# Kernel optimization log

Measured on AMD Instinct MI355X. Metric: run time of the kernel, lower is better.

The kernel has to match this reference:

```python
import jax, jax.numpy as jnp
import numpy as np

S, E, H, D, L = 2048, 1024, 16, 64, 6  # seq, embed(=H*D), heads, d_model, stack
FF = 4 * E
EPS = 1e-5


def _pos_embedding():
    pos = jnp.arange(S, dtype=jnp.float32)[:, None]
    idx = jnp.arange(E, dtype=jnp.float32)[None, :]
    ang = pos / jnp.power(10000.0, idx / E)
    # even positions -> sin row, odd positions -> cos row (as in the source)
    return jnp.where(jnp.arange(S)[:, None] % 2 == 0, jnp.sin(ang), jnp.cos(ang))


def _layer_norm(x, g, b):
    mu = jnp.mean(x, axis=-1, keepdims=True)
    var = jnp.mean(jnp.square(x - mu), axis=-1, keepdims=True)
    return (x - mu) * jax.lax.rsqrt(var + EPS) * g + b


def setup_inputs() -> dict:
    key = jax.random.key(0)
    ks = jax.random.split(key, 12)
    n = lambda k, shape, s=0.02: jax.random.normal(k, shape, jnp.float32) * s
    return {
        "x": jax.random.normal(ks[0], (S, E), jnp.float32),
        # shared (default-arg trap) input projections [d_model, embed]
        "Wk": n(ks[1], (D, E)), "Wq": n(ks[2], (D, E)), "Wv": n(ks[3], (D, E)),
        # per-layer per-head linears (stored [in,out])
        "hWk": n(ks[4], (L, H, D, D)), "hbk": jnp.zeros((L, H, D), jnp.float32),
        "hWq": n(ks[5], (L, H, D, D)), "hbq": jnp.zeros((L, H, D), jnp.float32),
        "hWv": n(ks[6], (L, H, D, D)), "hbv": jnp.zeros((L, H, D), jnp.float32),
        "Wo": n(ks[7], (L, E, E)), "bo": jnp.zeros((L, E), jnp.float32),
        "ln1_g": jnp.ones((L, E), jnp.float32), "ln1_b": jnp.zeros((L, E), jnp.float32),
        "W1": n(ks[8], (L, E, FF)), "b1": jnp.zeros((L, FF), jnp.float32),
        "W2": n(ks[9], (L, FF, E)), "b2": jnp.zeros((L, E), jnp.float32),
        "ln2_g": jnp.ones((L, E), jnp.float32), "ln2_b": jnp.zeros((L, E), jnp.float32),
    }


def reference(x, Wk, Wq, Wv, hWk, hbk, hWq, hbq, hWv, hbv, Wo, bo,
              ln1_g, ln1_b, W1, b1, W2, b2, ln2_g, ln2_b):
    h = x + _pos_embedding()
    scale = 1.0 / jnp.sqrt(jnp.float32(D))
    for l in range(L):
        # shared projections: [S, D]
        K = h @ Wk.T
        Q = h @ Wq.T
        V = h @ Wv.T
        # per-head linears: [H, S, D]
        kh = jnp.einsum('sd,hde->hse', K, hWk[l]) + hbk[l][:, None, :]
        qh = jnp.einsum('sd,hde->hse', Q, hWq[l]) + hbq[l][:, None, :]
        vh = jnp.einsum('sd,hde->hse', V, hWv[l]) + hbv[l][:, None, :]
        scores = jnp.einsum('hqd,hkd->hqk', qh, kh) * scale  # [H, S, S]
        attn = jax.nn.softmax(scores, axis=-1)
        out = jnp.einsum('hqk,hkd->hqd', attn, vh)           # [H, S, D]
        cat = jnp.transpose(out, (1, 0, 2)).reshape(S, H * D)  # [S, E]
        o = cat @ Wo[l] + bo[l]
        h = _layer_norm(o + h, ln1_g[l], ln1_b[l])
        # FFN
        f = jax.nn.relu(h @ W1[l] + b1[l]) @ W2[l] + b2[l]
        h = _layer_norm(f + h, ln2_g[l], ln2_b[l])
    return h
```

## Files before the change

### kernel.cpp

```cpp
#include <hip/hip_runtime.h>
#include <stdint.h>

typedef unsigned short u16;
typedef unsigned int   u32;

constexpr int SS = 2048, EE = 1024, HH = 16, DD = 64, LL = 6, FF = 4096;

typedef __bf16 bf16x8 __attribute__((ext_vector_type(8)));
typedef float  f32x4  __attribute__((ext_vector_type(4)));

#define DEV __device__ __forceinline__
#define AS1 __attribute__((address_space(1)))
#define AS3 __attribute__((address_space(3)))

DEV u16 f2bf(float f) {
    u32 u = __builtin_bit_cast(u32, f);
    u += 0x7FFFu + ((u >> 16) & 1u);
    return (u16)(u >> 16);
}

DEV float bf2f(u16 v) { return __builtin_bit_cast(float, (u32)v << 16); }

DEV void store_bf4(u16* p, float a, float b, float c, float d) {
    u32 lo = (u32)f2bf(a) | ((u32)f2bf(b) << 16);
    u32 hi = (u32)f2bf(c) | ((u32)f2bf(d) << 16);
    *(uint2*)p = make_uint2(lo, hi);
}

DEV void gload16(const void* g, void* l) {
    __builtin_amdgcn_global_load_lds((const AS1 void*)g, (AS3 void*)l, 16, 0, 0);
}

DEV f32x4 mfma16(bf16x8 a, bf16x8 b, f32x4 c) {
    return __builtin_amdgcn_mfma_f32_16x16x32_bf16(a, b, c, 0, 0, 0);
}

DEV float exp2_fast(float x) {
    float r;
    asm("v_exp_f32 %0, %1" : "=v"(r) : "v"(x));
    return r;
}

DEV int kvperm(int c) {
    return (c & 32) | ((c & 12) << 1) | ((c & 16) >> 2) | (c & 3);
}

DEV int xcd_swz(int flat, int nwg) {
    int chunk = nwg >> 3;
    return (flat & 7) * chunk + (flat >> 3);
}

constexpr size_t ALGN(size_t x) { return (x + 255) & ~(size_t)255; }
constexpr size_t OFF_WF   = 0;
constexpr size_t OFF_HWT  = ALGN(OFF_WF   + (size_t)3*LL*1024*1024*2);
constexpr size_t OFF_WSHT = ALGN(OFF_HWT  + (size_t)3*96*4096*2);
constexpr size_t OFF_HB   = ALGN(OFF_WSHT + (size_t)3*1024*64*2);
constexpr size_t OFF_WOT  = ALGN(OFF_HB   + (size_t)LL*3*HH*64*4);
constexpr size_t OFF_W1T  = ALGN(OFF_WOT  + (size_t)LL*EE*EE*2);
constexpr size_t OFF_W2T  = ALGN(OFF_W1T  + (size_t)LL*FF*EE*2);
constexpr size_t OFF_HBF  = ALGN(OFF_W2T  + (size_t)LL*EE*FF*2);
constexpr size_t OFF_QKVH = ALGN(OFF_HBF  + (size_t)SS*EE*2);
constexpr size_t OFF_VT   = OFF_QKVH + (size_t)2*HH*SS*64*2;
constexpr size_t OFF_CAT  = OFF_VT   + (size_t)1024*SS*2;
constexpr size_t OFF_F1   = OFF_QKVH;
constexpr size_t OFF_OF   = ALGN(OFF_CAT + (size_t)SS*EE*2);

__global__ void pos_add(const float* __restrict__ x, u16* __restrict__ hb) {
    const int row = blockIdx.x, tid = threadIdx.x;
    float4 x4 = ((const float4*)(x + (size_t)row * EE))[tid];
    float v[4] = {x4.x, x4.y, x4.z, x4.w};
    float y[4];
#pragma unroll
    for (int j = 0; j < 4; ++j) {
        int e = tid * 4 + j;
        float ang = (float)row * expf((float)e * (-9.210340371976184f / 1024.f));
        float pe = ((row & 1) == 0) ? sinf(ang) : cosf(ang);
        y[j] = v[j] + pe;
    }
    store_bf4(hb + (size_t)row * EE + tid * 4, y[0], y[1], y[2], y[3]);
}

__global__ void pack_bias(const float* __restrict__ bk, const float* __restrict__ bq,
                          const float* __restrict__ bv, float* __restrict__ dst) {
    int i = blockIdx.x * 256 + threadIdx.x;
    if (i >= LL * 3 * HH * 64) return;
    int d = i & 63;
    int hh = (i >> 6) & 15;
    int lt = i >> 10;
    int t = lt % 3, l = lt / 3;
    const float* s = (t == 0) ? bk : (t == 1) ? bq : bv;
    dst[i] = s[((size_t)l * HH + hh) * 64 + d];
}

DEV void tile_t64(const float* src, u16* dst, int R, int C, int c0, int r0,
                  float (*t)[65], int tid) {
    const int lr = tid >> 4, lc4 = (tid & 15) * 4;
#pragma unroll
    for (int i = 0; i < 4; ++i) {
        int r = i * 16 + lr;
        float4 v = *(const float4*)(src + (size_t)(r0 + r) * C + c0 + lc4);
        t[r][lc4] = v.x; t[r][lc4 + 1] = v.y; t[r][lc4 + 2] = v.z; t[r][lc4 + 3] = v.w;
    }
    __syncthreads();
    const int cr = tid >> 3, rr8 = (tid & 7) * 8;
#pragma unroll
    for (int i = 0; i < 2; ++i) {
        int cc = i * 32 + cr;
        u16 tmp[8];
#pragma unroll
        for (int j = 0; j < 8; ++j) tmp[j] = f2bf(t[rr8 + j][cc]);
        *(uint4*)(dst + (size_t)(c0 + cc) * R + r0 + rr8) = *(uint4*)tmp;
    }
}

__global__ void transpose_cast64(const float* __restrict__ src, u16* __restrict__ dst,
                                 int R, int C, long sSrc, long sDst) {
    __shared__ float t[64][65];
    const int b = blockIdx.z;
    tile_t64(src + (size_t)b * sSrc, dst + (size_t)b * sDst, R, C,
             blockIdx.x * 64, blockIdx.y * 64, t, threadIdx.x);
}

__global__ void hw_t3(const float* __restrict__ s0, const float* __restrict__ s1,
                      const float* __restrict__ s2, u16* __restrict__ dst) {
    __shared__ float t[64][65];
    const int z = blockIdx.z;
    const float* src = (z < 96 ? s0 : z < 192 ? s1 : s2) + (size_t)(z % 96) * 4096;
    tile_t64(src, dst + (size_t)z * 4096, 64, 64, 0, 0, t, threadIdx.x);
}

__global__ void wsh_t3(const float* __restrict__ s0, const float* __restrict__ s1,
                       const float* __restrict__ s2, u16* __restrict__ dst) {
    __shared__ float t[64][65];
    const int z = blockIdx.z;
    const float* src = (z == 0) ? s0 : (z == 1) ? s1 : s2;
    tile_t64(src, dst + (size_t)z * 65536, 64, 1024, blockIdx.x * 64, 0, t, threadIdx.x);
}

template<int BIASMODE, bool RELU, bool SPLITK, bool BATCH>
__launch_bounds__(256)
__global__ void gemm_std(const u16* __restrict__ A, const u16* __restrict__ B,
                         const float* __restrict__ bias, u16* __restrict__ Cb,
                         int M, int N, int K, int lda, int ldb,
                         long zsA, long zsB, long zsC) {
    __shared__ u16 As[2][128 * 64];
    __shared__ u16 Bs[2][128 * 64];
    const int gx = gridDim.x;
    const int swz = xcd_swz(blockIdx.y * gx + blockIdx.x, gx * gridDim.y);
    const int bn = swz % gx, bm = swz / gx, z = blockIdx.z;
    const int tid = threadIdx.x, w = tid >> 6;
    const int lane = tid & 63, l15 = lane & 15, hi = lane >> 4;
    const int wm = w >> 1, wn = w & 1;
    const u16* Ab = A + (size_t)bm * 128 * lda + (SPLITK ? (size_t)z * K : 0) + (BATCH ? (size_t)z * zsA : 0);
    const u16* Bb = B + (size_t)bn * 128 * ldb + (SPLITK ? (size_t)z * K : 0) + (BATCH ? (size_t)z * zsB : 0);
    const size_t coff = SPLITK ? (size_t)z * M * N : (BATCH ? (size_t)z * zsC : 0);
    const int tr = tid >> 3, tp = tid & 7;

    f32x4 acc[4][4];
#pragma unroll
    for (int i = 0; i < 4; ++i)
#pragma unroll
        for (int j = 0; j < 4; ++j) acc[i][j] = f32x4{0.f, 0.f, 0.f, 0.f};

    auto STAGE = [&](int b, int kt) {
        const u16* Abk = Ab + kt + (size_t)tr * lda + tp * 8;
        const u16* Bbk = Bb + kt + (size_t)tr * ldb + tp * 8;
#pragma unroll
        for (int i = 0; i < 4; ++i) {
            gload16(Abk + (size_t)i * 32 * lda, &As[b][(i * 256 + w * 64) * 8]);
            gload16(Bbk + (size_t)i * 32 * ldb, &Bs[b][(i * 256 + w * 64) * 8]);
        }
    };

    STAGE(0, 0);
    __syncthreads();
    int buf = 0;

    for (int kt = 0; kt < K; kt += 64) {
        if (kt + 64 < K) STAGE(buf ^ 1, kt + 64);
#pragma unroll
        for (int kk = 0; kk < 2; ++kk) {
            bf16x8 af[4], bf[4];
#pragma unroll
            for (int mi = 0; mi < 4; ++mi)
                af[mi] = *(const bf16x8*)&As[buf][(wm * 64 + mi * 16 + l15) * 64 + kk * 32 + hi * 8];
#pragma unroll
            for (int ni = 0; ni < 4; ++ni)
                bf[ni] = *(const bf16x8*)&Bs[buf][(wn * 64 + ni * 16 + l15) * 64 + kk * 32 + hi * 8];
#pragma unroll
            for (int mi = 0; mi < 4; ++mi)
#pragma unroll
                for (int ni = 0; ni < 4; ++ni)
                    acc[mi][ni] = mfma16(af[mi], bf[ni], acc[mi][ni]);
        }
        __syncthreads();
        buf ^= 1;
    }

#pragma unroll
    for (int mi = 0; mi < 4; ++mi) {
        int rg = bm * 128 + wm * 64 + mi * 16 + hi * 4;
#pragma unroll
        for (int ni = 0; ni < 4; ++ni) {
            int cg = bn * 128 + wn * 64 + ni * 16 + l15;
            float bc = (BIASMODE == 1) ? bias[cg] : 0.f;
#pragma unroll
            for (int r = 0; r < 4; ++r) {
                float v = acc[mi][ni][r] + bc;
                if (RELU) v = fmaxf(v, 0.f);
                Cb[coff + (size_t)(rg + r) * N + cg] = f2bf(v);
            }
        }
    }
}

__launch_bounds__(256)
__global__ void gemm_qkv(const u16* __restrict__ A, const u16* __restrict__ WF, int l,
                         const float* __restrict__ bias, u16* __restrict__ QKVH,
                         u16* __restrict__ VT) {
    __shared__ u16 As[2][128 * 64];
    __shared__ u16 Bs[2][128 * 64];
    const int gx = gridDim.x;
    const int swz = xcd_swz(blockIdx.y * gx + blockIdx.x, gx * gridDim.y);
    const int bn = swz % gx, bm = swz / gx;
    const int tid = threadIdx.x, w = tid >> 6;
    const int lane = tid & 63, l15 = lane & 15, hi = lane >> 4;
    const int wm = w >> 1, wn = w & 1;
    const int t = bn >> 3;
    const u16* Ab = A + (size_t)bm * 128 * 1024;
    const u16* Bb = WF + (((size_t)(t * 6 + l)) << 20) + (size_t)(bn & 7) * 128 * 1024;
    const int tr = tid >> 3, tp = tid & 7;

    f32x4 acc[4][4];
#pragma unroll
    for (int i = 0; i < 4; ++i)
#pragma unroll
        for (int j = 0; j < 4; ++j) acc[i][j] = f32x4{0.f, 0.f, 0.f, 0.f};

    auto STAGE = [&](int b, int kt) {
        const u16* Abk = Ab + kt + (size_t)tr * 1024 + tp * 8;
        const u16* Bbk = Bb + kt + (size_t)tr * 1024 + tp * 8;
#pragma unroll
        for (int i = 0; i < 4; ++i) {
            gload16(Abk + (size_t)i * 32 * 1024, &As[b][(i * 256 + w * 64) * 8]);
            gload16(Bbk + (size_t)i * 32 * 1024, &Bs[b][(i * 256 + w * 64) * 8]);
        }
    };

    STAGE(0, 0);
    __syncthreads();
    int buf = 0;

    for (int kt = 0; kt < 1024; kt += 64) {
        if (kt + 64 < 1024) STAGE(buf ^ 1, kt + 64);
#pragma unroll
        for (int kk = 0; kk < 2; ++kk) {
            bf16x8 af[4], bf[4];
#pragma unroll
            for (int mi = 0; mi < 4; ++mi)
                af[mi] = *(const bf16x8*)&As[buf][(wm * 64 + mi * 16 + l15) * 64 + kk * 32 + hi * 8];
#pragma unroll
            for (int ni = 0; ni < 4; ++ni)
                bf[ni] = *(const bf16x8*)&Bs[buf][(wn * 64 + ni * 16 + l15) * 64 + kk * 32 + hi * 8];
#pragma unroll
            for (int mi = 0; mi < 4; ++mi)
#pragma unroll
                for (int ni = 0; ni < 4; ++ni)
                    acc[mi][ni] = mfma16(af[mi], bf[ni], acc[mi][ni]);
        }
        __syncthreads();
        buf ^= 1;
    }

    if (t < 2) {
        const float sc = (t == 1) ? 0.18033688011112042f : 1.f;
#pragma unroll
        for (int mi = 0; mi < 4; ++mi) {
            int rg = bm * 128 + wm * 64 + mi * 16 + hi * 4;
#pragma unroll
            for (int ni = 0; ni < 4; ++ni) {
                int cg = bn * 128 + wn * 64 + ni * 16 + l15;
                int hd = cg & 1023, hh = hd >> 6, d = hd & 63;
                float bv = bias[cg];
                u16* dst = QKVH + (((size_t)(t * 16 + hh) * SS) + rg) * 64 + d;
#pragma unroll
                for (int r = 0; r < 4; ++r)
                    dst[(size_t)r * 64] = f2bf((acc[mi][ni][r] + bv) * sc);
            }
        }
    } else {
#pragma unroll
        for (int mi = 0; mi < 4; ++mi) {
            int s0 = bm * 128 + wm * 64 + mi * 16 + hi * 4;
            int ps = (s0 & ~63) | kvperm(s0 & 63);
#pragma unroll
            for (int ni = 0; ni < 4; ++ni) {
                int cg = bn * 128 + wn * 64 + ni * 16 + l15;
                int hd = cg & 1023;
                float bv = bias[cg];
                u16 tmp[4];
#pragma unroll
                for (int r = 0; r < 4; ++r) tmp[r] = f2bf(acc[mi][ni][r] + bv);
                *(uint2*)(VT + (size_t)hd * SS + ps) = *(uint2*)tmp;
            }
        }
    }
}

__launch_bounds__(256)
__global__ void attn_fwd(const u16* __restrict__ QKVH, const u16* __restrict__ VT,
                         u16* __restrict__ cat) {
    const int logical = (blockIdx.x & 7) * 64 + (blockIdx.x >> 3);
    const int h = logical >> 5, qt = logical & 31;
    const int tid = threadIdx.x, w = tid >> 6, lane = tid & 63;
    const int l15 = lane & 15, hi = lane >> 4;
    __shared__ u16 Ks[2][128 * 64];
    __shared__ u16 Vs[2][64 * 128];

    const u16* qb = QKVH + (((size_t)(16 + h) * SS) + qt * 64) * 64;
    const u16* kb = QKVH + ((size_t)h * SS) * 64;
    const u16* vb = VT + (size_t)h * 64 * SS;

    bf16x8 bq[2];
    {
        int qrow = w * 16 + l15;
        bq[0] = *(const bf16x8*)(qb + qrow * 64 + hi * 8);
        bq[1] = *(const bf16x8*)(qb + qrow * 64 + 32 + hi * 8);
    }
    bf16x8 ONES;
#pragma unroll
    for (int i = 0; i < 8; ++i) ONES[i] = (__bf16)1.0f;

    f32x4 oacc[4];
#pragma unroll
    for (int i = 0; i < 4; ++i) oacc[i] = f32x4{0.f, 0.f, 0.f, 0.f};
    f32x4 sacc = f32x4{0.f, 0.f, 0.f, 0.f};
    float mrun = 0.f;

    auto STAGE = [&](int buf, int t) {
#pragma unroll
        for (int j = 0; j < 4; ++j) {
            int fl = j * 256 + tid;
            int kr = fl >> 3, kc = (fl & 7) ^ (kr & 7);
            gload16(kb + ((size_t)(t * 128 + kr)) * 64 + kc * 8, &Ks[buf][fl * 8]);
            int vr = fl >> 4, vc = (fl & 15) ^ (vr & 7);
            gload16(vb + (size_t)vr * SS + t * 128 + vc * 8, &Vs[buf][fl * 8]);
        }
    };

    STAGE(0, 0);
    __syncthreads();
    int buf = 0;

    for (int t = 0; t < SS / 128; ++t) {
        if (t < SS / 128 - 1) STAGE(buf ^ 1, t + 1);
        const u16* ks = Ks[buf];
        const u16* vs = Vs[buf];

        f32x4 sc[8];
        __builtin_amdgcn_s_setprio(1);
#pragma unroll
        for (int mt = 0; mt < 8; ++mt) {
            int row = mt * 16 + l15;
            const u16* kr = ks + row * 64;
            f32x4 a = f32x4{0.f, 0.f, 0.f, 0.f};
            a = mfma16(*(const bf16x8*)&kr[((0 * 4 + hi) ^ (row & 7)) * 8], bq[0], a);
            a = mfma16(*(const bf16x8*)&kr[((1 * 4 + hi) ^ (row & 7)) * 8], bq[1], a);
            sc[mt] = a;
        }
        __builtin_amdgcn_s_setprio(0);

        bf16x8 pa[4];
#pragma unroll
        for (int ks2 = 0; ks2 < 4; ++ks2) {
            bf16x8 v;
#pragma unroll
            for (int r = 0; r < 4; ++r) {
                v[r]     = (__bf16)exp2_fast(sc[2 * ks2][r] - mrun);
                v[4 + r] = (__bf16)exp2_fast(sc[2 * ks2 + 1][r] - mrun);
            }
            pa[ks2] = v;
        }

        __builtin_amdgcn_s_setprio(1);
#pragma unroll
        for (int ks2 = 0; ks2 < 4; ++ks2) {
            sacc = mfma16(pa[ks2], ONES, sacc);
#pragma unroll
            for (int di = 0; di < 4; ++di) {
                int d = di * 16 + l15;
                bf16x8 bv = *(const bf16x8*)&vs[d * 128 + (((ks2 * 4 + hi) ^ (d & 7)) * 8)];
                oacc[di] = mfma16(pa[ks2], bv, oacc[di]);
            }
        }
        __builtin_amdgcn_s_setprio(0);

        float mx = fmaxf(fmaxf(sacc[0], sacc[1]), fmaxf(sacc[2], sacc[3]));
        if (__any(mx > 1.0e30f)) {
            const float dn = 5.421010862427522e-20f;
            mrun += 64.f;
#pragma unroll
            for (int r = 0; r < 4; ++r) sacc[r] *= dn;
#pragma unroll
            for (int di = 0; di < 4; ++di)
#pragma unroll
                for (int r = 0; r < 4; ++r) oacc[di][r] *= dn;
        }

        __syncthreads();
        buf ^= 1;
    }

#pragma unroll
    for (int di = 0; di < 4; ++di) {
        int col = h * 64 + di * 16 + l15;
#pragma unroll
        for (int r = 0; r < 4; ++r) {
            int row = qt * 64 + w * 16 + hi * 4 + r;
            cat[(size_t)row * EE + col] = f2bf(oacc[di][r] / sacc[r]);
        }
    }
}

template<bool FINAL>
__launch_bounds__(256)
__global__ void add_ln4(const u16* __restrict__ o, const float* __restrict__ ob,
                        const u16* __restrict__ res,
                        const float* __restrict__ g, const float* __restrict__ b,
                        float* __restrict__ fout, u16* __restrict__ hb) {
    const int row = blockIdx.x, tid = threadIdx.x;
    const int w = tid >> 6, lane = tid & 63;
    float x0, x1, x2, x3;
    {
        ushort4 r4 = ((const ushort4*)(res + (size_t)row * EE))[tid];
        float4 ob4 = ((const float4*)ob)[tid];
        x0 = bf2f(r4.x) + ob4.x; x1 = bf2f(r4.y) + ob4.y;
        x2 = bf2f(r4.z) + ob4.z; x3 = bf2f(r4.w) + ob4.w;
    }
#pragma unroll
    for (int z = 0; z < 4; ++z) {
        ushort4 a4 = ((const ushort4*)(o + (size_t)z * SS * EE + (size_t)row * EE))[tid];
        x0 += bf2f(a4.x); x1 += bf2f(a4.y); x2 += bf2f(a4.z); x3 += bf2f(a4.w);
    }
    float s = x0 + x1 + x2 + x3;
    float q = x0 * x0 + x1 * x1 + x2 * x2 + x3 * x3;
#pragma unroll
    for (int off = 1; off < 64; off <<= 1) { s += __shfl_xor(s, off); q += __shfl_xor(q, off); }
    __shared__ float red[8];
    if (lane == 0) { red[w] = s; red[4 + w] = q; }
    __syncthreads();
    s = red[0] + red[1] + red[2] + red[3];
    q = red[4] + red[5] + red[6] + red[7];
    const float mu = s * (1.f / EE);
    const float var = q * (1.f / EE) - mu * mu;
    const float rstd = rsqrtf(var + 1e-5f);
    const int c0 = tid * 4;
    float y0 = (x0 - mu) * rstd * g[c0 + 0] + b[c0 + 0];
    float y1 = (x1 - mu) * rstd * g[c0 + 1] + b[c0 + 1];
    float y2 = (x2 - mu) * rstd * g[c0 + 2] + b[c0 + 2];
    float y3 = (x3 - mu) * rstd * g[c0 + 3] + b[c0 + 3];
    if (FINAL) ((float4*)(fout + (size_t)row * EE))[tid] = make_float4(y0, y1, y2, y3);
    store_bf4(hb + (size_t)row * EE + c0, y0, y1, y2, y3);
}

extern "C" void kernel_launch(void* const* d_in, const int* in_sizes, int n_in,
                              void* d_out, int out_size, void* d_ws, size_t ws_size,
                              hipStream_t stream) {
    const float* x    = (const float*)d_in[0];
    const float* Wk   = (const float*)d_in[1];
    const float* Wq   = (const float*)d_in[2];
    const float* Wv   = (const float*)d_in[3];
    const float* hWk  = (const float*)d_in[4];
    const float* hbk  = (const float*)d_in[5];
    const float* hWq  = (const float*)d_in[6];
    const float* hbq  = (const float*)d_in[7];
    const float* hWv  = (const float*)d_in[8];
    const float* hbv  = (const float*)d_in[9];
    const float* Wo   = (const float*)d_in[10];
    const float* bo   = (const float*)d_in[11];
    const float* ln1g = (const float*)d_in[12];
    const float* ln1b = (const float*)d_in[13];
    const float* W1   = (const float*)d_in[14];
    const float* b1   = (const float*)d_in[15];
    const float* W2   = (const float*)d_in[16];
    const float* b2   = (const float*)d_in[17];
    const float* ln2g = (const float*)d_in[18];
    const float* ln2b = (const float*)d_in[19];

    char* ws = (char*)d_ws;
    u16*   WF   = (u16*)(ws + OFF_WF);
    u16*   HWT  = (u16*)(ws + OFF_HWT);
    u16*   WSHT = (u16*)(ws + OFF_WSHT);
    float* HB   = (float*)(ws + OFF_HB);
    u16*   WOT  = (u16*)(ws + OFF_WOT);
    u16*   W1T  = (u16*)(ws + OFF_W1T);
    u16*   W2T  = (u16*)(ws + OFF_W2T);
    u16*   HBF  = (u16*)(ws + OFF_HBF);
    u16*   QKVH = (u16*)(ws + OFF_QKVH);
    u16*   VT   = (u16*)(ws + OFF_VT);
    u16*   CAT  = (u16*)(ws + OFF_CAT);
    u16*   F1   = (u16*)(ws + OFF_F1);
    u16*   OFb  = (u16*)(ws + OFF_OF);

    pos_add<<<SS, 256, 0, stream>>>(x, HBF);
    pack_bias<<<72, 256, 0, stream>>>(hbk, hbq, hbv, HB);
    hw_t3<<<dim3(1, 1, 288), 256, 0, stream>>>(hWk, hWq, hWv, HWT);
    wsh_t3<<<dim3(16, 1, 3), 256, 0, stream>>>(Wk, Wq, Wv, WSHT);
    gemm_std<0, false, false, true><<<dim3(8, 48, 3), 256, 0, stream>>>(
        HWT, WSHT, nullptr, WF, 6144, 1024, 64, 64, 64,
        (long)96 * 4096, 65536, (long)6144 * 1024);
    transpose_cast64<<<dim3(16, 16, LL), 256, 0, stream>>>(Wo, WOT, EE, EE, (long)EE * EE, (long)EE * EE);
    transpose_cast64<<<dim3(64, 16, LL), 256, 0, stream>>>(W1, W1T, EE, FF, (long)EE * FF, (long)FF * EE);
    transpose_cast64<<<dim3(16, 64, LL), 256, 0, stream>>>(W2, W2T, FF, EE, (long)FF * EE, (long)EE * FF);

    for (int l = 0; l < LL; ++l) {
        gemm_qkv<<<dim3(24, 16, 1), 256, 0, stream>>>(HBF, WF, l, HB + (size_t)l * 3072, QKVH, VT);

        attn_fwd<<<512, 256, 0, stream>>>(QKVH, VT, CAT);

        gemm_std<0, false, true, false><<<dim3(8, 16, 4), 256, 0, stream>>>(
            CAT, WOT + (size_t)l * EE * EE, nullptr, OFb, SS, EE, 256, 1024, 1024, 0, 0, 0);
        add_ln4<false><<<SS, 256, 0, stream>>>(OFb, bo + (size_t)l * EE, HBF,
                                               ln1g + (size_t)l * EE, ln1b + (size_t)l * EE,
                                               nullptr, HBF);

        gemm_std<1, true, false, false><<<dim3(32, 16, 1), 256, 0, stream>>>(
            HBF, W1T + (size_t)l * FF * EE, b1 + (size_t)l * FF, F1, SS, FF, 1024, 1024, 1024, 0, 0, 0);
        gemm_std<0, false, true, false><<<dim3(8, 16, 4), 256, 0, stream>>>(
            F1, W2T + (size_t)l * EE * FF, nullptr, OFb, SS, EE, 1024, 4096, 4096, 0, 0, 0);
        if (l == LL - 1)
            add_ln4<true><<<SS, 256, 0, stream>>>(OFb, b2 + (size_t)l * EE, HBF,
                                                  ln2g + (size_t)l * EE, ln2b + (size_t)l * EE,
                                                  (float*)d_out, HBF);
        else
            add_ln4<false><<<SS, 256, 0, stream>>>(OFb, b2 + (size_t)l * EE, HBF,
                                                   ln2g + (size_t)l * EE, ln2b + (size_t)l * EE,
                                                   nullptr, HBF);
    }
}
```

Before: 940.8 us.

## Split attention KV tile across waves with cross-wave LDS reduction

The attention kernel now has each wave handle all 64 query rows against its own 32-key slice of each 128-key tile, instead of 16 query rows against all 128 keys. This cuts redundant K/V LDS reads per wave because each wave loads only its K and V fragments once per tile and reuses them across four query groups. At the end, per-wave partial outputs, row sums and running maxima are combined through shared memory. In exchange, accumulator registers grow fourfold (64 oacc values), which may lower occupancy, and a final reduction pass through LDS is added.

Result: no change. 930.8 us (-1.1%).

```diff
diff --git a/kernel.cpp b/kernel.cpp
--- a/kernel.cpp
+++ b/kernel.cpp
@@ -314,27 +314,30 @@
     const int h = logical >> 5, qt = logical & 31;
     const int tid = threadIdx.x, w = tid >> 6, lane = tid & 63;
     const int l15 = lane & 15, hi = lane >> 4;
-    __shared__ u16 Ks[2][128 * 64];
-    __shared__ u16 Vs[2][64 * 128];
+    __shared__ __align__(16) u16 smem[33824];
 
     const u16* qb = QKVH + (((size_t)(16 + h) * SS) + qt * 64) * 64;
     const u16* kb = QKVH + ((size_t)h * SS) * 64;
     const u16* vb = VT + (size_t)h * 64 * SS;
 
-    bf16x8 bq[2];
-    {
-        int qrow = w * 16 + l15;
-        bq[0] = *(const bf16x8*)(qb + qrow * 64 + hi * 8);
-        bq[1] = *(const bf16x8*)(qb + qrow * 64 + 32 + hi * 8);
+    bf16x8 bq[4][2];
+#pragma unroll
+    for (int qg = 0; qg < 4; ++qg) {
+        bq[qg][0] = *(const bf16x8*)(qb + (qg * 16 + l15) * 64 + hi * 8);
+        bq[qg][1] = *(const bf16x8*)(qb + (qg * 16 + l15) * 64 + 32 + hi * 8);
     }
     bf16x8 ONES;
 #pragma unroll
     for (int i = 0; i < 8; ++i) ONES[i] = (__bf16)1.0f;
 
-    f32x4 oacc[4];
-#pragma unroll
-    for (int i = 0; i < 4; ++i) oacc[i] = f32x4{0.f, 0.f, 0.f, 0.f};
-    f32x4 sacc = f32x4{0.f, 0.f, 0.f, 0.f};
+    f32x4 oacc[4][4];
+#pragma unroll
+    for (int i = 0; i < 4; ++i)
+#pragma unroll
+        for (int j = 0; j < 4; ++j) oacc[i][j] = f32x4{0.f, 0.f, 0.f, 0.f};
+    f32x4 sacc[4];
+#pragma unroll
+    for (int i = 0; i < 4; ++i) sacc[i] = f32x4{0.f, 0.f, 0.f, 0.f};
     float mrun = 0.f;
 
     auto STAGE = [&](int buf, int t) {
@@ -342,82 +345,140 @@
         for (int j = 0; j < 4; ++j) {
             int fl = j * 256 + tid;
             int kr = fl >> 3, kc = (fl & 7) ^ (kr & 7);
-            gload16(kb + ((size_t)(t * 128 + kr)) * 64 + kc * 8, &Ks[buf][fl * 8]);
+            gload16(kb + ((size_t)(t * 128 + kr)) * 64 + kc * 8, smem + buf * 8192 + fl * 8);
             int vr = fl >> 4, vc = (fl & 15) ^ (vr & 7);
-            gload16(vb + (size_t)vr * SS + t * 128 + vc * 8, &Vs[buf][fl * 8]);
+            gload16(vb + (size_t)vr * SS + t * 128 + vc * 8, smem + 16384 + buf * 8192 + fl * 8);
         }
     };
 
     STAGE(0, 0);
     __syncthreads();
     int buf = 0;
+    const int kbase = w * 32;
 
     for (int t = 0; t < SS / 128; ++t) {
         if (t < SS / 128 - 1) STAGE(buf ^ 1, t + 1);
-        const u16* ks = Ks[buf];
-        const u16* vs = Vs[buf];
-
-        f32x4 sc[8];
+        const u16* ks = smem + buf * 8192;
+        const u16* vs = smem + 16384 + buf * 8192;
+
+        bf16x8 kf[2][2];
+#pragma unroll
+        for (int kvg = 0; kvg < 2; ++kvg) {
+            int row = kbase + kvg * 16 + l15;
+            const u16* kr = ks + row * 64;
+            kf[kvg][0] = *(const bf16x8*)&kr[((0 * 4 + hi) ^ (row & 7)) * 8];
+            kf[kvg][1] = *(const bf16x8*)&kr[((1 * 4 + hi) ^ (row & 7)) * 8];
+        }
+
+        f32x4 sc[4][2];
         __builtin_amdgcn_s_setprio(1);
 #pragma unroll
-        for (int mt = 0; mt < 8; ++mt) {
-            int row = mt * 16 + l15;
-            const u16* kr = ks + row * 64;
-            f32x4 a = f32x4{0.f, 0.f, 0.f, 0.f};
-            a = mfma16(*(const bf16x8*)&kr[((0 * 4 + hi) ^ (row & 7)) * 8], bq[0], a);
-            a = mfma16(*(const bf16x8*)&kr[((1 * 4 + hi) ^ (row & 7)) * 8], bq[1], a);
-            sc[mt] = a;
-        }
+        for (int qg = 0; qg < 4; ++qg)
+#pragma unroll
+            for (int kvg = 0; kvg < 2; ++kvg) {
+                f32x4 a = f32x4{0.f, 0.f, 0.f, 0.f};
+                a = mfma16(kf[kvg][0], bq[qg][0], a);
+                a = mfma16(kf[kvg][1], bq[qg][1], a);
+                sc[qg][kvg] = a;
+            }
         __builtin_amdgcn_s_setprio(0);
 
         bf16x8 pa[4];
 #pragma unroll
-        for (int ks2 = 0; ks2 < 4; ++ks2) {
+        for (int qg = 0; qg < 4; ++qg) {
             bf16x8 v;
 #pragma unroll
             for (int r = 0; r < 4; ++r) {
-                v[r]     = (__bf16)exp2_fast(sc[2 * ks2][r] - mrun);
-                v[4 + r] = (__bf16)exp2_fast(sc[2 * ks2 + 1][r] - mrun);
+                v[r]     = (__bf16)exp2_fast(sc[qg][0][r] - mrun);
+                v[4 + r] = (__bf16)exp2_fast(sc[qg][1][r] - mrun);
             }
-            pa[ks2] = v;
+            pa[qg] = v;
+        }
+
+        bf16x8 bv[4];
+#pragma unroll
+        for (int di = 0; di < 4; ++di) {
+            int d = di * 16 + l15;
+            bv[di] = *(const bf16x8*)&vs[d * 128 + (((w * 4 + hi) ^ (d & 7)) * 8)];
         }
 
         __builtin_amdgcn_s_setprio(1);
 #pragma unroll
-        for (int ks2 = 0; ks2 < 4; ++ks2) {
-            sacc = mfma16(pa[ks2], ONES, sacc);
-#pragma unroll
-            for (int di = 0; di < 4; ++di) {
-                int d = di * 16 + l15;
-                bf16x8 bv = *(const bf16x8*)&vs[d * 128 + (((ks2 * 4 + hi) ^ (d & 7)) * 8)];
-                oacc[di] = mfma16(pa[ks2], bv, oacc[di]);
-            }
+        for (int qg = 0; qg < 4; ++qg) {
+            sacc[qg] = mfma16(pa[qg], ONES, sacc[qg]);
+#pragma unroll
+            for (int di = 0; di < 4; ++di)
+                oacc[qg][di] = mfma16(pa[qg], bv[di], oacc[qg][di]);
         }
         __builtin_amdgcn_s_setprio(0);
 
-        float mx = fmaxf(fmaxf(sacc[0], sacc[1]), fmaxf(sacc[2], sacc[3]));
+        float mx = sacc[0][0];
+#pragma unroll
+        for (int qg = 0; qg < 4; ++qg)
+#pragma unroll
+            for (int r = 0; r < 4; ++r) mx = fmaxf(mx, sacc[qg][r]);
         if (__any(mx > 1.0e30f)) {
             const float dn = 5.421010862427522e-20f;
             mrun += 64.f;
 #pragma unroll
-            for (int r = 0; r < 4; ++r) sacc[r] *= dn;
-#pragma unroll
-            for (int di = 0; di < 4; ++di)
-#pragma unroll
-                for (int r = 0; r < 4; ++r) oacc[di][r] *= dn;
+            for (int qg = 0; qg < 4; ++qg) {
+#pragma unroll
+                for (int r = 0; r < 4; ++r) sacc[qg][r] *= dn;
+#pragma unroll
+                for (int di = 0; di < 4; ++di)
+#pragma unroll
+                    for (int r = 0; r < 4; ++r) oacc[qg][di][r] *= dn;
+            }
         }
 
         __syncthreads();
         buf ^= 1;
     }
 
+    float* P4   = (float*)smem;
+    float* sred = P4 + 4 * 64 * 65;
+    float* smr  = sred + 4 * 64;
+#pragma unroll
+    for (int qg = 0; qg < 4; ++qg) {
+        int q = qg * 16 + hi * 4;
+#pragma unroll
+        for (int di = 0; di < 4; ++di)
+#pragma unroll
+            for (int r = 0; r < 4; ++r)
+                P4[(size_t)(w * 64 + q + r) * 65 + di * 16 + l15] = oacc[qg][di][r];
+        if (l15 == 0) {
+#pragma unroll
+            for (int r = 0; r < 4; ++r) sred[w * 64 + q + r] = sacc[qg][r];
+        }
+    }
+    if (lane == 0) smr[w] = mrun;
+    __syncthreads();
+
+    float mmax = fmaxf(fmaxf(smr[0], smr[1]), fmaxf(smr[2], smr[3]));
+    float wsc[4];
+#pragma unroll
+    for (int sw = 0; sw < 4; ++sw) wsc[sw] = exp2_fast(smr[sw] - mmax);
+
+    float rs[4];
+#pragma unroll
+    for (int r = 0; r < 4; ++r) {
+        int q = w * 16 + hi * 4 + r;
+        float s = 0.f;
+#pragma unroll
+        for (int sw = 0; sw < 4; ++sw) s += sred[sw * 64 + q] * wsc[sw];
+        rs[r] = 1.f / s;
+    }
 #pragma unroll
     for (int di = 0; di < 4; ++di) {
         int col = h * 64 + di * 16 + l15;
 #pragma unroll
         for (int r = 0; r < 4; ++r) {
-            int row = qt * 64 + w * 16 + hi * 4 + r;
-            cat[(size_t)row * EE + col] = f2bf(oacc[di][r] / sacc[r]);
+            int q = w * 16 + hi * 4 + r;
+            float o = 0.f;
+#pragma unroll
+            for (int sw = 0; sw < 4; ++sw)
+                o += P4[(size_t)(sw * 64 + q) * 65 + di * 16 + l15] * wsc[sw];
+            cat[(size_t)(qt * 64 + q) * EE + col] = f2bf(o * rs[r]);
         }
     }
 }
```
